# Kernel optimization log

Measured on AMD Instinct MI355X. Metric: run time of the kernel, lower is better.

The kernel has to match this reference:

```python
import jax, jax.numpy as jnp
import numpy as np

B, K, D, DS = 32, 64, 4, 4
H = 512            # hidden_dim
HH = H // 2        # hidden_hidden_dim = 256
NA = 2             # n_action


def _lin(k, out_d, in_d):
    kw, kb = jax.random.split(k)
    w = jax.random.normal(kw, (out_d, in_d), dtype=jnp.float32) * (in_d ** -0.5)
    b = jax.random.normal(kb, (out_d,), dtype=jnp.float32) * 0.01
    return w, b


def setup_inputs() -> dict:
    key = jax.random.key(0)
    ks = jax.random.split(key, 16)
    state = jax.random.normal(ks[0], (B, DS), dtype=jnp.float32)
    obs = jax.random.normal(ks[1], (B, D, K), dtype=jnp.float32)
    layer_w, layer_b = _lin(ks[2], H, DS)
    e1_w, e1_b = _lin(ks[3], H, 2 * D)
    e2_w, e2_b = _lin(ks[4], H, H)
    e3_w, e3_b = _lin(ks[5], H, H)
    ln_g = jnp.ones((H,), jnp.float32)
    ln_b = jnp.zeros((H,), jnp.float32)
    n1_w, n1_b = _lin(ks[6], H, D + H + DS)
    n2_w, n2_b = _lin(ks[7], HH, H)
    mu1_w, mu1_b = _lin(ks[8], 256, H + H)
    mu2_w, mu2_b = _lin(ks[9], 128, 256)
    mu3_w, mu3_b = _lin(ks[10], NA, 128)
    s1_w, s1_b = _lin(ks[11], 256, H + H)
    s2_w, s2_b = _lin(ks[12], 128, 256)
    s3_w, s3_b = _lin(ks[13], NA, 128)
    return dict(state=state, obs=obs, layer_w=layer_w, layer_b=layer_b,
                e1_w=e1_w, e1_b=e1_b, e2_w=e2_w, e2_b=e2_b, e3_w=e3_w, e3_b=e3_b,
                ln_g=ln_g, ln_b=ln_b, n1_w=n1_w, n1_b=n1_b, n2_w=n2_w, n2_b=n2_b,
                mu1_w=mu1_w, mu1_b=mu1_b, mu2_w=mu2_w, mu2_b=mu2_b, mu3_w=mu3_w, mu3_b=mu3_b,
                s1_w=s1_w, s1_b=s1_b, s2_w=s2_w, s2_b=s2_b, s3_w=s3_w, s3_b=s3_b)


def _dense(x, w, b):
    return x @ w.T + b


def reference(state, obs, layer_w, layer_b, e1_w, e1_b, e2_w, e2_b, e3_w, e3_b,
              ln_g, ln_b, n1_w, n1_b, n2_w, n2_b,
              mu1_w, mu1_b, mu2_w, mu2_b, mu3_w, mu3_b,
              s1_w, s1_b, s2_w, s2_b, s3_w, s3_b):
    # ---- InteractionNetwork ----
    o = jnp.transpose(obs, (0, 2, 1))                       # [B,K,D]
    mask = jnp.sum(jnp.abs(o), axis=2) != 0                 # [B,K] bool
    counts = jnp.clip(jnp.sum(mask, axis=1, keepdims=True).astype(o.dtype), 1e-6)  # [B,1]
    # all-pairs edge features [B,K,K,2D]
    obs_i = jnp.broadcast_to(o[:, :, None, :], (B, K, K, D))
    obs_j = jnp.broadcast_to(o[:, None, :, :], (B, K, K, D))
    edge_input = jnp.concatenate([obs_i, obs_j], axis=-1)
    h = jax.nn.relu(_dense(edge_input, e1_w, e1_b))
    h = jax.nn.relu(_dense(h, e2_w, e2_b))
    edge_output = jax.nn.relu(_dense(h, e3_w, e3_b))        # [B,K,K,H]
    edge_mask = (mask[:, :, None] & mask[:, None, :]).astype(o.dtype)  # [B,K,K]
    edge_output = edge_output * edge_mask[..., None]
    valid_counts = jnp.clip(jnp.sum(edge_mask, axis=2, keepdims=True), 1e-6)  # [B,K,1]
    agg = jnp.sum(edge_output, axis=2) / valid_counts       # [B,K,H]
    # LayerNorm (eps=1e-5, torch default)
    mu_ = jnp.mean(agg, axis=-1, keepdims=True)
    var_ = jnp.mean((agg - mu_) ** 2, axis=-1, keepdims=True)
    agg = (agg - mu_) * jax.lax.rsqrt(var_ + 1e-5) * ln_g + ln_b
    st_exp = jnp.broadcast_to(state[:, None, :], (B, K, DS))
    node_input = jnp.concatenate([o, agg, st_exp], axis=-1)  # [B,K,D+H+DS]
    node_output = _dense(jax.nn.relu(_dense(node_input, n1_w, n1_b)), n2_w, n2_b)  # [B,K,HH]
    m3 = mask[:, :, None]
    mean_pool = jnp.sum(jnp.where(m3, node_output, 0.0), axis=1) / counts  # [B,HH]
    max_pool = jnp.max(jnp.where(m3, node_output, -1e9), axis=1)           # [B,HH]
    obs_feat = jnp.concatenate([mean_pool, max_pool], axis=-1)             # [B,H]
    # ---- ActorNetwork head ----
    st_feat = jax.nn.relu(_dense(state, layer_w, layer_b))                 # [B,H]
    x = jnp.concatenate([st_feat, obs_feat], axis=1)                       # [B,2H]
    mu = _dense(jax.nn.relu(_dense(jax.nn.relu(_dense(x, mu1_w, mu1_b)), mu2_w, mu2_b)), mu3_w, mu3_b)
    std = jax.nn.softplus(_dense(jax.nn.relu(_dense(jax.nn.relu(_dense(x, s1_w, s1_b)), s2_w, s2_b)), s3_w, s3_b))
    std = jnp.clip(std + 0.001, 0.1, 2.0)
    return mu, std
```

## Files before the change

### kernel.cpp

```cpp
#include <hip/hip_runtime.h>
#include <hip/hip_fp16.h>

typedef _Float16 f16x8 __attribute__((ext_vector_type(8)));
typedef _Float16 f16x4 __attribute__((ext_vector_type(4)));
typedef float f32x4 __attribute__((ext_vector_type(4)));

#define NB 32
#define NK 64
#define ND 4
#define NH 512
#define NKP 544
#define RTOT 131072


__global__ void prep_obs_kernel(const float* __restrict__ obs,
                                const float* __restrict__ state,
                                float* __restrict__ o,
                                float* __restrict__ maskp,
                                float* __restrict__ cntp,
                                _Float16* __restrict__ nodein) {
  const int b = blockIdx.x;
  const int j = threadIdx.x;
  float o0 = obs[(b*4 + 0)*64 + j];
  float o1 = obs[(b*4 + 1)*64 + j];
  float o2 = obs[(b*4 + 2)*64 + j];
  float o3 = obs[(b*4 + 3)*64 + j];
  size_t bi = (size_t)b*64 + j;
  float* orow = o + bi*4;
  orow[0] = o0; orow[1] = o1; orow[2] = o2; orow[3] = o3;
  float s = fabsf(o0) + fabsf(o1) + fabsf(o2) + fabsf(o3);
  float m = (s != 0.0f) ? 1.0f : 0.0f;
  maskp[bi] = m;
  float c = m;
  #pragma unroll
  for (int off = 1; off < 64; off <<= 1) c += __shfl_xor(c, off);
  if (j == 0) cntp[b] = fmaxf(c, 1e-6f);
  _Float16* nrow = nodein + bi*NKP;
  nrow[0] = (_Float16)o0; nrow[1] = (_Float16)o1;
  nrow[2] = (_Float16)o2; nrow[3] = (_Float16)o3;
  nrow[516] = (_Float16)state[b*4 + 0];
  nrow[517] = (_Float16)state[b*4 + 1];
  nrow[518] = (_Float16)state[b*4 + 2];
  nrow[519] = (_Float16)state[b*4 + 3];
  for (int k2 = 520; k2 < 544; ++k2) nrow[k2] = (_Float16)0.0f;
}

__global__ void prep_uv16(const float* __restrict__ o,
                          const float* __restrict__ e1w,
                          const float* __restrict__ e1b,
                          _Float16* __restrict__ u16,
                          _Float16* __restrict__ v16) {
  const int bi = blockIdx.x;
  const int c = threadIdx.x;
  const float* orow = o + (size_t)bi*4;
  float o0 = orow[0], o1 = orow[1], o2 = orow[2], o3 = orow[3];
  const float* wr = e1w + c*8;
  float u = wr[0]*o0 + wr[1]*o1 + wr[2]*o2 + wr[3]*o3 + e1b[c];
  float v = wr[4]*o0 + wr[5]*o1 + wr[6]*o2 + wr[7]*o3;
  u16[(size_t)bi*NH + c] = (_Float16)u;
  v16[(size_t)bi*NH + c] = (_Float16)v;
}

__global__ void prep_w16_kernel(const float* __restrict__ e2w,
                                const float* __restrict__ e3w,
                                const float* __restrict__ n2w,
                                const float* __restrict__ n1w,
                                _Float16* __restrict__ w2h,
                                _Float16* __restrict__ w3h,
                                _Float16* __restrict__ n2wh,
                                _Float16* __restrict__ n1wh) {
  int idx = blockIdx.x * blockDim.x + threadIdx.x;
  const int A = 512*512, Bc = 512*512, C = 256*512, Dn = 512*544;
  if (idx < A) {
    w2h[idx] = (_Float16)e2w[idx];
  } else if (idx < A + Bc) {
    int q = idx - A; w3h[q] = (_Float16)e3w[q];
  } else if (idx < A + Bc + C) {
    int q = idx - A - Bc; n2wh[q] = (_Float16)n2w[q];
  } else if (idx < A + Bc + C + Dn) {
    int q = idx - A - Bc - C;
    int n = q / 544, k = q % 544;
    n1wh[q] = (k < 520) ? (_Float16)n1w[n*520 + k] : (_Float16)0.0f;
  }
}

__global__ void prep_stfeat_kernel(const float* __restrict__ state,
                                   const float* __restrict__ lw,
                                   const float* __restrict__ lb,
                                   float* __restrict__ xfeat) {
  const int b = blockIdx.x, c = threadIdx.x;
  const float* s = state + b*4;
  const float* wr = lw + c*4;
  float hv = wr[0]*s[0] + wr[1]*s[1] + wr[2]*s[2] + wr[3]*s[3] + lb[c];
  xfeat[b*1024 + c] = fmaxf(hv, 0.0f);
}


__global__ __launch_bounds__(512, 2) void edge_fused(
    const _Float16* __restrict__ u16, const _Float16* __restrict__ v16,
    const _Float16* __restrict__ w2h, const _Float16* __restrict__ w3h,
    const float* __restrict__ e2b, const float* __restrict__ e3b,
    const float* __restrict__ maskp, const float* __restrict__ cntp,
    float* __restrict__ agg) {
  __shared__ __align__(16) char lds[131072];
  __shared__ float em_s[64];

  const int t = threadIdx.x;
  const int bi0 = blockIdx.x * 2;
  const int b = bi0 >> 6;
  const int w = t >> 6, l = t & 63, lr = l & 15, lg = l >> 4;
  const int wcol = w * 64;

  if (t < 64) em_s[t] = maskp[(size_t)b*64 + t];

  {
    const int tr = t >> 3;
    const int kc = t & 7;
    const _Float16* vrow = v16 + ((size_t)(b*64 + tr))*NH + kc*64;
    const _Float16* u0p  = u16 + (size_t)bi0*NH + kc*64;
    const _Float16* u1p  = u16 + (size_t)(bi0 + 1)*NH + kc*64;
    #pragma unroll
    for (int e8 = 0; e8 < 8; ++e8) {
      f16x8 vv = *(const f16x8*)(vrow + e8*8);
      f16x8 u0 = *(const f16x8*)(u0p + e8*8);
      f16x8 u1 = *(const f16x8*)(u1p + e8*8);
      f16x8 h0, h1;
      #pragma unroll
      for (int e = 0; e < 8; ++e) {
        _Float16 x0 = u0[e] + vv[e];
        _Float16 x1 = u1[e] + vv[e];
        h0[e] = x0 > (_Float16)0 ? x0 : (_Float16)0;
        h1[e] = x1 > (_Float16)0 ? x1 : (_Float16)0;
      }
      const int k16 = (kc*8 + e8)*16;
      *(f16x8*)(lds + ((tr*1024 + k16) ^ ((tr & 7) << 4))) = h0;
      *(f16x8*)(lds + (((64 + tr)*1024 + k16) ^ ((tr & 7) << 4))) = h1;
    }
  }
  __syncthreads();

  f32x4 acc[8][4];

  {
    #pragma unroll
    for (int nt = 0; nt < 4; ++nt) {
      float bz = e2b[wcol + nt*16 + lr];
      #pragma unroll
      for (int mt = 0; mt < 8; ++mt) {
        acc[mt][nt][0] = bz; acc[mt][nt][1] = bz;
        acc[mt][nt][2] = bz; acc[mt][nt][3] = bz;
      }
    }
    const _Float16* bbase = w2h + (size_t)(wcol + lr)*NH + lg*8;
    f16x8 bfp[4];
    #pragma unroll
    for (int nt = 0; nt < 4; ++nt)
      bfp[nt] = *(const f16x8*)(bbase + nt*16*NH);
    for (int kk = 0; kk < 16; ++kk) {
      f16x8 bf[4];
      #pragma unroll
      for (int nt = 0; nt < 4; ++nt) bf[nt] = bfp[nt];
      if (kk < 15) {
        #pragma unroll
        for (int nt = 0; nt < 4; ++nt)
          bfp[nt] = *(const f16x8*)(bbase + nt*16*NH + (kk+1)*32);
      }
      const int k16 = (kk*4 + lg)*16;
      #pragma unroll
      for (int mt = 0; mt < 8; ++mt) {
        int row = mt*16 + lr;
        f16x8 af = *(const f16x8*)(lds + ((row*1024 + k16) ^ ((row & 7) << 4)));
        #pragma unroll
        for (int nt = 0; nt < 4; ++nt)
          acc[mt][nt] = __builtin_amdgcn_mfma_f32_16x16x32_f16(af, bf[nt], acc[mt][nt], 0, 0, 0);
      }
    }
  }
  __syncthreads();

  #pragma unroll
  for (int mt = 0; mt < 8; ++mt)
    #pragma unroll
    for (int nt = 0; nt < 4; ++nt)
      #pragma unroll
      for (int r = 0; r < 4; ++r) {
        int row = mt*16 + lg*4 + r;
        int cc = wcol + nt*16 + lr;
        *(_Float16*)(lds + ((row*1024 + cc*2) ^ ((row & 7) << 4))) =
            (_Float16)fmaxf(acc[mt][nt][r], 0.0f);
      }
  __syncthreads();

  {
    #pragma unroll
    for (int nt = 0; nt < 4; ++nt) {
      float bz = e3b[wcol + nt*16 + lr];
      #pragma unroll
      for (int mt = 0; mt < 8; ++mt) {
        acc[mt][nt][0] = bz; acc[mt][nt][1] = bz;
        acc[mt][nt][2] = bz; acc[mt][nt][3] = bz;
      }
    }
    const _Float16* bbase = w3h + (size_t)(wcol + lr)*NH + lg*8;
    f16x8 bfp[4];
    #pragma unroll
    for (int nt = 0; nt < 4; ++nt)
      bfp[nt] = *(const f16x8*)(bbase + nt*16*NH);
    for (int kk = 0; kk < 16; ++kk) {
      f16x8 bf[4];
      #pragma unroll
      for (int nt = 0; nt < 4; ++nt) bf[nt] = bfp[nt];
      if (kk < 15) {
        #pragma unroll
        for (int nt = 0; nt < 4; ++nt)
          bfp[nt] = *(const f16x8*)(bbase + nt*16*NH + (kk+1)*32);
      }
      const int k16 = (kk*4 + lg)*16;
      #pragma unroll
      for (int mt = 0; mt < 8; ++mt) {
        int row = mt*16 + lr;
        f16x8 af = *(const f16x8*)(lds + ((row*1024 + k16) ^ ((row & 7) << 4)));
        #pragma unroll
        for (int nt = 0; nt < 4; ++nt)
          acc[mt][nt] = __builtin_amdgcn_mfma_f32_16x16x32_f16(af, bf[nt], acc[mt][nt], 0, 0, 0);
      }
    }
  }

  float csum[2][4] = {{0.f,0.f,0.f,0.f},{0.f,0.f,0.f,0.f}};
  #pragma unroll
  for (int mt = 0; mt < 8; ++mt) {
    const int g = mt >> 2;
    float em0 = em_s[(mt&3)*16 + lg*4 + 0];
    float em1 = em_s[(mt&3)*16 + lg*4 + 1];
    float em2 = em_s[(mt&3)*16 + lg*4 + 2];
    float em3 = em_s[(mt&3)*16 + lg*4 + 3];
    #pragma unroll
    for (int nt = 0; nt < 4; ++nt) {
      csum[g][nt] += em0 * fmaxf(acc[mt][nt][0], 0.f)
                   + em1 * fmaxf(acc[mt][nt][1], 0.f)
                   + em2 * fmaxf(acc[mt][nt][2], 0.f)
                   + em3 * fmaxf(acc[mt][nt][3], 0.f);
    }
  }
  #pragma unroll
  for (int g = 0; g < 2; ++g)
    #pragma unroll
    for (int nt = 0; nt < 4; ++nt) {
      csum[g][nt] += __shfl_xor(csum[g][nt], 16);
      csum[g][nt] += __shfl_xor(csum[g][nt], 32);
    }
  float cnt = cntp[b];
  if (lg == 0) {
    #pragma unroll
    for (int g = 0; g < 2; ++g) {
      int big = bi0 + g;
      float sc = em_s[big & 63] / cnt;
      #pragma unroll
      for (int nt = 0; nt < 4; ++nt)
        agg[(size_t)big*NH + wcol + nt*16 + lr] = csum[g][nt] * sc;
    }
  }
}

__global__ __launch_bounds__(256) void ln_kernel(
    const float* __restrict__ agg, const float* __restrict__ lng,
    const float* __restrict__ lnb, _Float16* __restrict__ nodein) {
  const int w = threadIdx.x >> 6, l = threadIdx.x & 63;
  const int row = blockIdx.x*4 + w;
  const float* ar = agg + (size_t)row*NH + l*8;
  float4 a0 = *(const float4*)ar;
  float4 a1 = *(const float4*)(ar + 4);
  float s1 = a0.x + a0.y + a0.z + a0.w + a1.x + a1.y + a1.z + a1.w;
  float s2 = a0.x*a0.x + a0.y*a0.y + a0.z*a0.z + a0.w*a0.w
           + a1.x*a1.x + a1.y*a1.y + a1.z*a1.z + a1.w*a1.w;
  #pragma unroll
  for (int off = 1; off < 64; off <<= 1) {
    s1 += __shfl_xor(s1, off);
    s2 += __shfl_xor(s2, off);
  }
  float mean = s1 * (1.0f/512.0f);
  float rstd = rsqrtf(s2 * (1.0f/512.0f) - mean*mean + 1e-5f);
  float4 g0 = *(const float4*)(lng + l*8);
  float4 g1 = *(const float4*)(lng + l*8 + 4);
  float4 b0 = *(const float4*)(lnb + l*8);
  float4 b1 = *(const float4*)(lnb + l*8 + 4);
  f16x4 o0, o1;
  o0[0] = (_Float16)((a0.x - mean) * rstd * g0.x + b0.x);
  o0[1] = (_Float16)((a0.y - mean) * rstd * g0.y + b0.y);
  o0[2] = (_Float16)((a0.z - mean) * rstd * g0.z + b0.z);
  o0[3] = (_Float16)((a0.w - mean) * rstd * g0.w + b0.w);
  o1[0] = (_Float16)((a1.x - mean) * rstd * g1.x + b1.x);
  o1[1] = (_Float16)((a1.y - mean) * rstd * g1.y + b1.y);
  o1[2] = (_Float16)((a1.z - mean) * rstd * g1.z + b1.z);
  o1[3] = (_Float16)((a1.w - mean) * rstd * g1.w + b1.w);
  _Float16* nr = nodein + (size_t)row*NKP + 4 + l*8;
  *(f16x4*)nr = o0;
  *(f16x4*)(nr + 4) = o1;
}


template <int RELU16>
__global__ __launch_bounds__(256) void node_gemm(
    const _Float16* __restrict__ A, const _Float16* __restrict__ Bw,
    const float* __restrict__ bias, void* __restrict__ outp,
    int Ka, int ldo) {
  const int t = threadIdx.x;
  const int w = t >> 6, l = t & 63, lr = l & 15, lg = l >> 4;
  const int m0 = blockIdx.x * 64;
  const int col = blockIdx.y * 64 + w*16 + lr;
  f32x4 acc[4];
  float bz = bias[col];
  #pragma unroll
  for (int mt = 0; mt < 4; ++mt) {
    acc[mt][0] = bz; acc[mt][1] = bz; acc[mt][2] = bz; acc[mt][3] = bz;
  }
  const _Float16* bptr = Bw + (size_t)col*Ka + lg*8;
  const _Float16* aptr = A + (size_t)(m0 + lr)*Ka + lg*8;
  const int nkk = Ka >> 5;
  for (int kk = 0; kk < nkk; ++kk) {
    f16x8 bf = *(const f16x8*)(bptr + kk*32);
    #pragma unroll
    for (int mt = 0; mt < 4; ++mt) {
      f16x8 af = *(const f16x8*)(aptr + ((size_t)mt*16)*Ka + kk*32);
      acc[mt] = __builtin_amdgcn_mfma_f32_16x16x32_f16(af, bf, acc[mt], 0, 0, 0);
    }
  }
  #pragma unroll
  for (int mt = 0; mt < 4; ++mt)
    #pragma unroll
    for (int r = 0; r < 4; ++r) {
      int row = m0 + mt*16 + lg*4 + r;
      float vv = acc[mt][r];
      if (RELU16)
        ((_Float16*)outp)[(size_t)row*ldo + col] = (_Float16)fmaxf(vv, 0.f);
      else
        ((float*)outp)[(size_t)row*ldo + col] = vv;
    }
}


__global__ __launch_bounds__(256) void pool_kernel(
    const float* __restrict__ nodeout, const float* __restrict__ maskp,
    const float* __restrict__ cntp, float* __restrict__ xfeat) {
  const int b = blockIdx.x;
  const int c = threadIdx.x;
  float sum = 0.f, mx = -1e9f;
  for (int i = 0; i < 64; ++i) {
    float m = maskp[b*64 + i];
    float v = nodeout[((size_t)(b*64 + i))*256 + c];
    sum += m * v;
    mx = fmaxf(mx, (m != 0.f) ? v : -1e9f);
  }
  xfeat[b*1024 + 512 + c] = sum / cntp[b];
  xfeat[b*1024 + 768 + c] = mx;
}

__global__ __launch_bounds__(256) void heads_g1(
    const float* __restrict__ xfeat,
    const float* __restrict__ mu1w, const float* __restrict__ s1w,
    float* __restrict__ part) {
  __shared__ __align__(16) float xs[256];
  const int b = blockIdx.x, h = blockIdx.y, ks = blockIdx.z;
  const int t = threadIdx.x;
  xs[t] = xfeat[b*1024 + ks*256 + t];
  __syncthreads();
  const float* wr = (h ? s1w : mu1w) + (size_t)t*1024 + ks*256;
  float a = 0.f;
  #pragma unroll 8
  for (int k = 0; k < 256; k += 4) {
    float4 ww = *(const float4*)(wr + k);
    float4 xx = *(const float4*)(xs + k);
    a += ww.x*xx.x + ww.y*xx.y + ww.z*xx.z + ww.w*xx.w;
  }
  part[(((size_t)(b*2 + h))*256 + t)*4 + ks] = a;
}

__global__ __launch_bounds__(256) void heads_g23(
    const float* __restrict__ part,
    const float* __restrict__ mu1b, const float* __restrict__ s1b,
    const float* __restrict__ mu2w, const float* __restrict__ mu2b,
    const float* __restrict__ s2w, const float* __restrict__ s2b,
    const float* __restrict__ mu3w, const float* __restrict__ mu3b,
    const float* __restrict__ s3w, const float* __restrict__ s3b,
    float* __restrict__ outp) {
  __shared__ __align__(16) float h1s[256];
  __shared__ __align__(16) float h2s[128];
  const int b = blockIdx.x, h = blockIdx.y;
  const int t = threadIdx.x;
  {
    float4 pp = *(const float4*)(part + (((size_t)(b*2 + h))*256 + t)*4);
    float a = pp.x + pp.y + pp.z + pp.w + (h ? s1b : mu1b)[t];
    h1s[t] = fmaxf(a, 0.f);
  }
  __syncthreads();
  {
    const int o = t >> 1, half = t & 1;
    const float* wr = (h ? s2w : mu2w) + (size_t)o*256 + half*128;
    const float* hp = h1s + half*128;
    float a = 0.f;
    #pragma unroll 8
    for (int k = 0; k < 128; k += 4) {
      float4 ww = *(const float4*)(wr + k);
      float4 hh = *(const float4*)(hp + k);
      a += ww.x*hh.x + ww.y*hh.y + ww.z*hh.z + ww.w*hh.w;
    }
    a += __shfl_xor(a, 1);
    if (half == 0) h2s[o] = fmaxf(a + (h ? s2b : mu2b)[o], 0.f);
  }
  __syncthreads();
  if (t < 64) {
    const int o = t >> 5, lane = t & 31;
    const float* wr = (h ? s3w : mu3w) + o*128 + lane*4;
    const float* hp = h2s + lane*4;
    float4 ww = *(const float4*)wr;
    float4 hh = *(const float4*)hp;
    float a = ww.x*hh.x + ww.y*hh.y + ww.z*hh.z + ww.w*hh.w;
    #pragma unroll
    for (int off = 1; off < 32; off <<= 1) a += __shfl_xor(a, off);
    if (lane == 0) {
      a += (h ? s3b : mu3b)[o];
      if (h == 0) {
        outp[b*2 + o] = a;
      } else {
        float spv = (a > 0.f) ? (a + log1pf(expf(-a))) : log1pf(expf(a));
        outp[64 + b*2 + o] = fminf(fmaxf(spv + 0.001f, 0.1f), 2.0f);
      }
    }
  }
}


extern "C" void kernel_launch(void* const* d_in, const int* in_sizes, int n_in,
                              void* d_out, int out_size, void* d_ws, size_t ws_size,
                              hipStream_t stream) {
  const float* state  = (const float*)d_in[0];
  const float* obs    = (const float*)d_in[1];
  const float* layerw = (const float*)d_in[2];
  const float* layerb = (const float*)d_in[3];
  const float* e1w    = (const float*)d_in[4];
  const float* e1b    = (const float*)d_in[5];
  const float* e2w    = (const float*)d_in[6];
  const float* e2b    = (const float*)d_in[7];
  const float* e3w    = (const float*)d_in[8];
  const float* e3b    = (const float*)d_in[9];
  const float* lng    = (const float*)d_in[10];
  const float* lnb    = (const float*)d_in[11];
  const float* n1w    = (const float*)d_in[12];
  const float* n1b    = (const float*)d_in[13];
  const float* n2w    = (const float*)d_in[14];
  const float* n2b    = (const float*)d_in[15];
  const float* mu1w   = (const float*)d_in[16];
  const float* mu1b   = (const float*)d_in[17];
  const float* mu2w   = (const float*)d_in[18];
  const float* mu2b   = (const float*)d_in[19];
  const float* mu3w   = (const float*)d_in[20];
  const float* mu3b   = (const float*)d_in[21];
  const float* s1w    = (const float*)d_in[22];
  const float* s1b    = (const float*)d_in[23];
  const float* s2w    = (const float*)d_in[24];
  const float* s2b    = (const float*)d_in[25];
  const float* s3w    = (const float*)d_in[26];
  const float* s3b    = (const float*)d_in[27];
  float* outp = (float*)d_out;

  char* p = (char*)d_ws;
  auto alloc = [&](size_t bytes) {
    char* r = p;
    p += (bytes + 255) & ~(size_t)255;
    return r;
  };
  float*    o       = (float*)alloc((size_t)2048*4*4);
  float*    maskp   = (float*)alloc((size_t)2048*4);
  float*    cntp    = (float*)alloc((size_t)32*4);
  _Float16* u16     = (_Float16*)alloc((size_t)2048*512*2);
  _Float16* v16     = (_Float16*)alloc((size_t)2048*512*2);
  _Float16* w2h     = (_Float16*)alloc((size_t)512*512*2);
  _Float16* w3h     = (_Float16*)alloc((size_t)512*512*2);
  _Float16* nodein  = (_Float16*)alloc((size_t)2048*544*2);
  _Float16* n1wh    = (_Float16*)alloc((size_t)512*544*2);
  _Float16* n2wh    = (_Float16*)alloc((size_t)256*512*2);
  _Float16* nodeh   = (_Float16*)alloc((size_t)2048*512*2);
  float*    nodeout = (float*)alloc((size_t)2048*256*4);
  float*    xfeat   = (float*)alloc((size_t)32*1024*4);
  float*    agg     = (float*)alloc((size_t)2048*512*4);
  float*    hpart   = (float*)alloc((size_t)32*2*256*4*4);

  prep_obs_kernel<<<32, 64, 0, stream>>>(obs, state, o, maskp, cntp, nodein);
  prep_uv16<<<2048, 512, 0, stream>>>(o, e1w, e1b, u16, v16);
  prep_w16_kernel<<<3648, 256, 0, stream>>>(e2w, e3w, n2w, n1w, w2h, w3h, n2wh, n1wh);
  prep_stfeat_kernel<<<32, 512, 0, stream>>>(state, layerw, layerb, xfeat);

  edge_fused<<<1024, 512, 0, stream>>>(u16, v16, w2h, w3h, e2b, e3b,
                                       maskp, cntp, agg);
  ln_kernel<<<512, 256, 0, stream>>>(agg, lng, lnb, nodein);

  node_gemm<1><<<dim3(32, 8), 256, 0, stream>>>(nodein, n1wh, n1b, (void*)nodeh, 544, 512);
  node_gemm<0><<<dim3(32, 4), 256, 0, stream>>>(nodeh, n2wh, n2b, (void*)nodeout, 512, 256);
  pool_kernel<<<32, 256, 0, stream>>>(nodeout, maskp, cntp, xfeat);
  heads_g1<<<dim3(32, 2, 4), 256, 0, stream>>>(xfeat, mu1w, s1w, hpart);
  heads_g23<<<dim3(32, 2), 256, 0, stream>>>(hpart, mu1b, s1b, mu2w, mu2b,
                                             s2w, s2b, mu3w, mu3b, s3w, s3b, outp);
}
```

Before: 237.4 us.

## Fuse layernorm into edge kernel with one node per block, swapped MFMA operands

The edge MLP kernel now handles one (b,i) node per block instead of two. This halves LDS to 64KB and allows 4 blocks per CU. The MFMA operands are swapped so weights are the A operand and edge rows the B operand, which lets the j-reduction use lane shuffles. The layernorm is fused into the kernel epilogue, removing the fp32 agg buffer round trip and the separate ln_kernel launch. The cost is that each weight tile is reloaded from global or L2 twice as often per block, with more blocks and more syncs.

```diff
diff --git a/kernel.cpp b/kernel.cpp
--- a/kernel.cpp
+++ b/kernel.cpp
@@ -10,7 +10,6 @@
 #define ND 4
 #define NH 512
 #define NKP 544
-#define RTOT 131072
 
 
 __global__ void prep_obs_kernel(const float* __restrict__ obs,
@@ -96,207 +95,193 @@
 }
 
 
-__global__ __launch_bounds__(512, 2) void edge_fused(
+__global__ __launch_bounds__(512, 4) void edge_fused(
     const _Float16* __restrict__ u16, const _Float16* __restrict__ v16,
     const _Float16* __restrict__ w2h, const _Float16* __restrict__ w3h,
     const float* __restrict__ e2b, const float* __restrict__ e3b,
     const float* __restrict__ maskp, const float* __restrict__ cntp,
-    float* __restrict__ agg) {
-  __shared__ __align__(16) char lds[131072];
+    const float* __restrict__ lng, const float* __restrict__ lnb,
+    _Float16* __restrict__ nodein) {
+  __shared__ __align__(16) char lds[65536];
   __shared__ float em_s[64];
+  __shared__ float red_s[16];
+  __shared__ float stat_s[2];
 
   const int t = threadIdx.x;
-  const int bi0 = blockIdx.x * 2;
-  const int b = bi0 >> 6;
+  const int bi = blockIdx.x;
+  const int b = bi >> 6;
+  const int iq = bi & 63;
   const int w = t >> 6, l = t & 63, lr = l & 15, lg = l >> 4;
   const int wcol = w * 64;
 
   if (t < 64) em_s[t] = maskp[(size_t)b*64 + t];
 
   {
-    const int tr = t >> 3;
+    const int row = t >> 3;
     const int kc = t & 7;
-    const _Float16* vrow = v16 + ((size_t)(b*64 + tr))*NH + kc*64;
-    const _Float16* u0p  = u16 + (size_t)bi0*NH + kc*64;
-    const _Float16* u1p  = u16 + (size_t)(bi0 + 1)*NH + kc*64;
+    const _Float16* vrow = v16 + ((size_t)(b*64 + row))*NH + kc*64;
+    const _Float16* urow = u16 + (size_t)bi*NH + kc*64;
     #pragma unroll
     for (int e8 = 0; e8 < 8; ++e8) {
       f16x8 vv = *(const f16x8*)(vrow + e8*8);
-      f16x8 u0 = *(const f16x8*)(u0p + e8*8);
-      f16x8 u1 = *(const f16x8*)(u1p + e8*8);
-      f16x8 h0, h1;
+      f16x8 uu = *(const f16x8*)(urow + e8*8);
+      f16x8 hv;
       #pragma unroll
       for (int e = 0; e < 8; ++e) {
-        _Float16 x0 = u0[e] + vv[e];
-        _Float16 x1 = u1[e] + vv[e];
-        h0[e] = x0 > (_Float16)0 ? x0 : (_Float16)0;
-        h1[e] = x1 > (_Float16)0 ? x1 : (_Float16)0;
-      }
-      const int k16 = (kc*8 + e8)*16;
-      *(f16x8*)(lds + ((tr*1024 + k16) ^ ((tr & 7) << 4))) = h0;
-      *(f16x8*)(lds + (((64 + tr)*1024 + k16) ^ ((tr & 7) << 4))) = h1;
-    }
-  }
-  __syncthreads();
-
-  f32x4 acc[8][4];
+        _Float16 x = uu[e] + vv[e];
+        hv[e] = x > (_Float16)0 ? x : (_Float16)0;
+      }
+      *(f16x8*)(lds + ((row*1024 + (kc*64 + e8*8)*2) ^ ((row & 7) << 4))) = hv;
+    }
+  }
+  __syncthreads();
+
+  f32x4 acc[4][4];
 
   {
     #pragma unroll
     for (int nt = 0; nt < 4; ++nt) {
-      float bz = e2b[wcol + nt*16 + lr];
-      #pragma unroll
-      for (int mt = 0; mt < 8; ++mt) {
-        acc[mt][nt][0] = bz; acc[mt][nt][1] = bz;
-        acc[mt][nt][2] = bz; acc[mt][nt][3] = bz;
-      }
-    }
-    const _Float16* bbase = w2h + (size_t)(wcol + lr)*NH + lg*8;
-    f16x8 bfp[4];
+      float4 bz = *(const float4*)(e2b + wcol + nt*16 + lg*4);
+      #pragma unroll
+      for (int jt = 0; jt < 4; ++jt) {
+        acc[jt][nt][0] = bz.x; acc[jt][nt][1] = bz.y;
+        acc[jt][nt][2] = bz.z; acc[jt][nt][3] = bz.w;
+      }
+    }
+    const _Float16* abase = w2h + (size_t)(wcol + lr)*NH + lg*8;
+    f16x8 afp[4];
     #pragma unroll
     for (int nt = 0; nt < 4; ++nt)
-      bfp[nt] = *(const f16x8*)(bbase + nt*16*NH);
+      afp[nt] = *(const f16x8*)(abase + nt*16*NH);
     for (int kk = 0; kk < 16; ++kk) {
-      f16x8 bf[4];
-      #pragma unroll
-      for (int nt = 0; nt < 4; ++nt) bf[nt] = bfp[nt];
+      f16x8 af[4];
+      #pragma unroll
+      for (int nt = 0; nt < 4; ++nt) af[nt] = afp[nt];
       if (kk < 15) {
         #pragma unroll
         for (int nt = 0; nt < 4; ++nt)
-          bfp[nt] = *(const f16x8*)(bbase + nt*16*NH + (kk+1)*32);
-      }
-      const int k16 = (kk*4 + lg)*16;
-      #pragma unroll
-      for (int mt = 0; mt < 8; ++mt) {
-        int row = mt*16 + lr;
-        f16x8 af = *(const f16x8*)(lds + ((row*1024 + k16) ^ ((row & 7) << 4)));
+          afp[nt] = *(const f16x8*)(abase + nt*16*NH + (kk+1)*32);
+      }
+      #pragma unroll
+      for (int jt = 0; jt < 4; ++jt) {
+        const int j = jt*16 + lr;
+        f16x8 bf = *(const f16x8*)(lds + ((j*1024 + kk*64 + lg*16) ^ ((j & 7) << 4)));
         #pragma unroll
         for (int nt = 0; nt < 4; ++nt)
-          acc[mt][nt] = __builtin_amdgcn_mfma_f32_16x16x32_f16(af, bf[nt], acc[mt][nt], 0, 0, 0);
-      }
-    }
-  }
-  __syncthreads();
-
-  #pragma unroll
-  for (int mt = 0; mt < 8; ++mt)
+          acc[jt][nt] = __builtin_amdgcn_mfma_f32_16x16x32_f16(af[nt], bf, acc[jt][nt], 0, 0, 0);
+      }
+    }
+  }
+  __syncthreads();
+
+  #pragma unroll
+  for (int jt = 0; jt < 4; ++jt) {
+    const int j = jt*16 + lr;
+    #pragma unroll
+    for (int nt = 0; nt < 4; ++nt) {
+      f16x4 hv;
+      #pragma unroll
+      for (int r = 0; r < 4; ++r)
+        hv[r] = (_Float16)fmaxf(acc[jt][nt][r], 0.0f);
+      *(f16x4*)(lds + ((j*1024 + (wcol + nt*16 + lg*4)*2) ^ ((j & 7) << 4))) = hv;
+    }
+  }
+  __syncthreads();
+
+  {
+    #pragma unroll
+    for (int nt = 0; nt < 4; ++nt) {
+      float4 bz = *(const float4*)(e3b + wcol + nt*16 + lg*4);
+      #pragma unroll
+      for (int jt = 0; jt < 4; ++jt) {
+        acc[jt][nt][0] = bz.x; acc[jt][nt][1] = bz.y;
+        acc[jt][nt][2] = bz.z; acc[jt][nt][3] = bz.w;
+      }
+    }
+    const _Float16* abase = w3h + (size_t)(wcol + lr)*NH + lg*8;
+    f16x8 afp[4];
     #pragma unroll
     for (int nt = 0; nt < 4; ++nt)
-      #pragma unroll
-      for (int r = 0; r < 4; ++r) {
-        int row = mt*16 + lg*4 + r;
-        int cc = wcol + nt*16 + lr;
-        *(_Float16*)(lds + ((row*1024 + cc*2) ^ ((row & 7) << 4))) =
-            (_Float16)fmaxf(acc[mt][nt][r], 0.0f);
-      }
-  __syncthreads();
-
-  {
-    #pragma unroll
-    for (int nt = 0; nt < 4; ++nt) {
-      float bz = e3b[wcol + nt*16 + lr];
-      #pragma unroll
-      for (int mt = 0; mt < 8; ++mt) {
-        acc[mt][nt][0] = bz; acc[mt][nt][1] = bz;
-        acc[mt][nt][2] = bz; acc[mt][nt][3] = bz;
-      }
-    }
-    const _Float16* bbase = w3h + (size_t)(wcol + lr)*NH + lg*8;
-    f16x8 bfp[4];
-    #pragma unroll
-    for (int nt = 0; nt < 4; ++nt)
-      bfp[nt] = *(const f16x8*)(bbase + nt*16*NH);
+      afp[nt] = *(const f16x8*)(abase + nt*16*NH);
     for (int kk = 0; kk < 16; ++kk) {
-      f16x8 bf[4];
-      #pragma unroll
-      for (int nt = 0; nt < 4; ++nt) bf[nt] = bfp[nt];
+      f16x8 af[4];
+      #pragma unroll
+      for (int nt = 0; nt < 4; ++nt) af[nt] = afp[nt];
       if (kk < 15) {
         #pragma unroll
         for (int nt = 0; nt < 4; ++nt)
-          bfp[nt] = *(const f16x8*)(bbase + nt*16*NH + (kk+1)*32);
-      }
-      const int k16 = (kk*4 + lg)*16;
-      #pragma unroll
-      for (int mt = 0; mt < 8; ++mt) {
-        int row = mt*16 + lr;
-        f16x8 af = *(const f16x8*)(lds + ((row*1024 + k16) ^ ((row & 7) << 4)));
+          afp[nt] = *(const f16x8*)(abase + nt*16*NH + (kk+1)*32);
+      }
+      #pragma unroll
+      for (int jt = 0; jt < 4; ++jt) {
+        const int j = jt*16 + lr;
+        f16x8 bf = *(const f16x8*)(lds + ((j*1024 + kk*64 + lg*16) ^ ((j & 7) << 4)));
         #pragma unroll
         for (int nt = 0; nt < 4; ++nt)
-          acc[mt][nt] = __builtin_amdgcn_mfma_f32_16x16x32_f16(af, bf[nt], acc[mt][nt], 0, 0, 0);
-      }
-    }
-  }
-
-  float csum[2][4] = {{0.f,0.f,0.f,0.f},{0.f,0.f,0.f,0.f}};
-  #pragma unroll
-  for (int mt = 0; mt < 8; ++mt) {
-    const int g = mt >> 2;
-    float em0 = em_s[(mt&3)*16 + lg*4 + 0];
-    float em1 = em_s[(mt&3)*16 + lg*4 + 1];
-    float em2 = em_s[(mt&3)*16 + lg*4 + 2];
-    float em3 = em_s[(mt&3)*16 + lg*4 + 3];
+          acc[jt][nt] = __builtin_amdgcn_mfma_f32_16x16x32_f16(af[nt], bf, acc[jt][nt], 0, 0, 0);
+      }
+    }
+  }
+
+  float csum[4][4];
+  #pragma unroll
+  for (int nt = 0; nt < 4; ++nt)
+    #pragma unroll
+    for (int r = 0; r < 4; ++r) csum[nt][r] = 0.0f;
+  #pragma unroll
+  for (int jt = 0; jt < 4; ++jt) {
+    float em = em_s[jt*16 + lr];
+    #pragma unroll
+    for (int nt = 0; nt < 4; ++nt)
+      #pragma unroll
+      for (int r = 0; r < 4; ++r)
+        csum[nt][r] += em * fmaxf(acc[jt][nt][r], 0.0f);
+  }
+  #pragma unroll
+  for (int nt = 0; nt < 4; ++nt)
+    #pragma unroll
+    for (int r = 0; r < 4; ++r) {
+      csum[nt][r] += __shfl_xor(csum[nt][r], 1);
+      csum[nt][r] += __shfl_xor(csum[nt][r], 2);
+      csum[nt][r] += __shfl_xor(csum[nt][r], 4);
+      csum[nt][r] += __shfl_xor(csum[nt][r], 8);
+    }
+  float scale = em_s[iq] / cntp[b];
+
+  __syncthreads();
+  float* aggs = (float*)lds;
+  if (lr == 0) {
     #pragma unroll
     for (int nt = 0; nt < 4; ++nt) {
-      csum[g][nt] += em0 * fmaxf(acc[mt][nt][0], 0.f)
-                   + em1 * fmaxf(acc[mt][nt][1], 0.f)
-                   + em2 * fmaxf(acc[mt][nt][2], 0.f)
-                   + em3 * fmaxf(acc[mt][nt][3], 0.f);
-    }
-  }
-  #pragma unroll
-  for (int g = 0; g < 2; ++g)
-    #pragma unroll
-    for (int nt = 0; nt < 4; ++nt) {
-      csum[g][nt] += __shfl_xor(csum[g][nt], 16);
-      csum[g][nt] += __shfl_xor(csum[g][nt], 32);
-    }
-  float cnt = cntp[b];
-  if (lg == 0) {
-    #pragma unroll
-    for (int g = 0; g < 2; ++g) {
-      int big = bi0 + g;
-      float sc = em_s[big & 63] / cnt;
-      #pragma unroll
-      for (int nt = 0; nt < 4; ++nt)
-        agg[(size_t)big*NH + wcol + nt*16 + lr] = csum[g][nt] * sc;
-    }
-  }
-}
-
-__global__ __launch_bounds__(256) void ln_kernel(
-    const float* __restrict__ agg, const float* __restrict__ lng,
-    const float* __restrict__ lnb, _Float16* __restrict__ nodein) {
-  const int w = threadIdx.x >> 6, l = threadIdx.x & 63;
-  const int row = blockIdx.x*4 + w;
-  const float* ar = agg + (size_t)row*NH + l*8;
-  float4 a0 = *(const float4*)ar;
-  float4 a1 = *(const float4*)(ar + 4);
-  float s1 = a0.x + a0.y + a0.z + a0.w + a1.x + a1.y + a1.z + a1.w;
-  float s2 = a0.x*a0.x + a0.y*a0.y + a0.z*a0.z + a0.w*a0.w
-           + a1.x*a1.x + a1.y*a1.y + a1.z*a1.z + a1.w*a1.w;
+      float4 av;
+      av.x = csum[nt][0] * scale; av.y = csum[nt][1] * scale;
+      av.z = csum[nt][2] * scale; av.w = csum[nt][3] * scale;
+      *(float4*)(aggs + wcol + nt*16 + lg*4) = av;
+    }
+  }
+  __syncthreads();
+
+  float a = aggs[t];
+  float s1 = a, s2 = a * a;
   #pragma unroll
   for (int off = 1; off < 64; off <<= 1) {
     s1 += __shfl_xor(s1, off);
     s2 += __shfl_xor(s2, off);
   }
-  float mean = s1 * (1.0f/512.0f);
-  float rstd = rsqrtf(s2 * (1.0f/512.0f) - mean*mean + 1e-5f);
-  float4 g0 = *(const float4*)(lng + l*8);
-  float4 g1 = *(const float4*)(lng + l*8 + 4);
-  float4 b0 = *(const float4*)(lnb + l*8);
-  float4 b1 = *(const float4*)(lnb + l*8 + 4);
-  f16x4 o0, o1;
-  o0[0] = (_Float16)((a0.x - mean) * rstd * g0.x + b0.x);
-  o0[1] = (_Float16)((a0.y - mean) * rstd * g0.y + b0.y);
-  o0[2] = (_Float16)((a0.z - mean) * rstd * g0.z + b0.z);
-  o0[3] = (_Float16)((a0.w - mean) * rstd * g0.w + b0.w);
-  o1[0] = (_Float16)((a1.x - mean) * rstd * g1.x + b1.x);
-  o1[1] = (_Float16)((a1.y - mean) * rstd * g1.y + b1.y);
-  o1[2] = (_Float16)((a1.z - mean) * rstd * g1.z + b1.z);
-  o1[3] = (_Float16)((a1.w - mean) * rstd * g1.w + b1.w);
-  _Float16* nr = nodein + (size_t)row*NKP + 4 + l*8;
-  *(f16x4*)nr = o0;
-  *(f16x4*)(nr + 4) = o1;
+  if (l == 0) { red_s[w] = s1; red_s[8 + w] = s2; }
+  __syncthreads();
+  if (t == 0) {
+    float S1 = 0.f, S2 = 0.f;
+    #pragma unroll
+    for (int q = 0; q < 8; ++q) { S1 += red_s[q]; S2 += red_s[8 + q]; }
+    float mean = S1 * (1.0f/512.0f);
+    float var = S2 * (1.0f/512.0f) - mean * mean;
+    stat_s[0] = mean;
+    stat_s[1] = rsqrtf(var + 1e-5f);
+  }
+  __syncthreads();
+  float nrm = (a - stat_s[0]) * stat_s[1] * lng[t] + lnb[t];
+  nodein[(size_t)bi*NKP + 4 + t] = (_Float16)nrm;
 }
 
 
@@ -483,7 +468,6 @@
   _Float16* nodeh   = (_Float16*)alloc((size_t)2048*512*2);
   float*    nodeout = (float*)alloc((size_t)2048*256*4);
   float*    xfeat   = (float*)alloc((size_t)32*1024*4);
-  float*    agg     = (float*)alloc((size_t)2048*512*4);
   float*    hpart   = (float*)alloc((size_t)32*2*256*4*4);
 
   prep_obs_kernel<<<32, 64, 0, stream>>>(obs, state, o, maskp, cntp, nodein);
@@ -491,9 +475,8 @@
   prep_w16_kernel<<<3648, 256, 0, stream>>>(e2w, e3w, n2w, n1w, w2h, w3h, n2wh, n1wh);
   prep_stfeat_kernel<<<32, 512, 0, stream>>>(state, layerw, layerb, xfeat);
 
-  edge_fused<<<1024, 512, 0, stream>>>(u16, v16, w2h, w3h, e2b, e3b,
-                                       maskp, cntp, agg);
-  ln_kernel<<<512, 256, 0, stream>>>(agg, lng, lnb, nodein);
+  edge_fused<<<2048, 512, 0, stream>>>(u16, v16, w2h, w3h, e2b, e3b,
+                                       maskp, cntp, lng, lnb, nodein);
 
   node_gemm<1><<<dim3(32, 8), 256, 0, stream>>>(nodein, n1wh, n1b, (void*)nodeh, 544, 512);
   node_gemm<0><<<dim3(32, 4), 256, 0, stream>>>(nodeh, n2wh, n2b, (void*)nodeout, 512, 256);
```

After: 376.2 us. +58.4%, slower.
